# Kernel tuning notes

Measured on AMD Instinct MI355X. Metric: run time of the kernel, lower is better.

## Reference

```python
import jax, jax.numpy as jnp
import numpy as np


def grid_sample_bilinear(feat, grid):
    """Bilinear grid_sample, align_corners=False, zeros padding.
    feat: [B, C, H, W]; grid: [B, N, 2] with (x, y) in [-1, 1]. Returns [B, C, N].
    """
    B, C, H, W = feat.shape
    gx, gy = grid[..., 0], grid[..., 1]
    # unnormalize (align_corners=False): pixel = ((g + 1) * size - 1) / 2
    ix = ((gx + 1.0) * W - 1.0) * 0.5
    iy = ((gy + 1.0) * H - 1.0) * 0.5
    x0 = jnp.floor(ix)
    y0 = jnp.floor(iy)
    x1 = x0 + 1.0
    y1 = y0 + 1.0
    wx1 = ix - x0
    wx0 = 1.0 - wx1
    wy1 = iy - y0
    wy0 = 1.0 - wy1
    featf = feat.reshape(B, C, H * W)

    def corner(xi, yi, w):
        valid = (xi >= 0) & (xi <= W - 1) & (yi >= 0) & (yi <= H - 1)
        xi_c = jnp.clip(xi, 0, W - 1).astype(jnp.int32)
        yi_c = jnp.clip(yi, 0, H - 1).astype(jnp.int32)
        idx = yi_c * W + xi_c                                  # [B, N]
        vals = jnp.take_along_axis(featf, idx[:, None, :], axis=2)  # [B, C, N]
        return vals * (w * valid.astype(feat.dtype))[:, None, :]

    return (corner(x0, y0, wx0 * wy0) + corner(x1, y0, wx1 * wy0)
            + corner(x0, y1, wx0 * wy1) + corner(x1, y1, wx1 * wy1))


def setup_inputs() -> dict:
    key = jax.random.key(0)
    ks = jax.random.split(key, 8)
    B_T, C, H, W = 128, 256, 64, 64
    J = 17
    n_heads, n_points = 8, 4
    HP = n_heads * n_points
    video_features = jax.random.normal(ks[0], (B_T, C, H, W), dtype=jnp.float32)
    reference_points = jax.random.uniform(ks[1], (B_T, J, 2), dtype=jnp.float32,
                                          minval=-1.0, maxval=1.0)
    # offset predictor: Linear(C -> HP*2); weights init small like the module
    W_off = 0.01 * jax.random.normal(ks[2], (C, HP * 2), dtype=jnp.float32)
    b_off = 0.01 * jax.random.normal(ks[3], (HP * 2,), dtype=jnp.float32)
    # weight predictor: Linear(C -> HP)
    W_w = 0.01 * jax.random.normal(ks[4], (C, HP), dtype=jnp.float32)
    b_w = jnp.zeros((HP,), dtype=jnp.float32)
    # output projection: Linear(C -> C), xavier-ish scale
    W_out = jax.random.normal(ks[5], (C, C), dtype=jnp.float32) * (1.0 / np.sqrt(C))
    b_out = jnp.zeros((C,), dtype=jnp.float32)
    return {"video_features": video_features, "reference_points": reference_points,
            "W_off": W_off, "b_off": b_off, "W_w": W_w, "b_w": b_w,
            "W_out": W_out, "b_out": b_out}


def reference(video_features, reference_points, W_off, b_off, W_w, b_w, W_out, b_out):
    B, C, H, W = video_features.shape
    J = reference_points.shape[1]
    HP = W_w.shape[1]  # n_heads * n_points
    # initial queries: sample features at reference points -> [B, J, C]
    q = grid_sample_bilinear(video_features, reference_points).transpose(0, 2, 1)
    # learned fractional offsets: [B, J, HP, 2]
    offsets = (q @ W_off + b_off).reshape(B, J, HP, 2)
    # softmax attention weights over all heads*points: [B, J, HP]
    weights = jax.nn.softmax(q @ W_w + b_w, axis=-1)
    # final sampling grid, clamped to valid range: [B, J*HP, 2]
    grid = jnp.clip(reference_points[:, :, None, :] + offsets, -1.0, 1.0)
    grid = grid.reshape(B, J * HP, 2)
    # sample and weighted-sum: [B, C, J, HP] x [B, J, HP] -> [B, J, C]
    sampled = grid_sample_bilinear(video_features, grid).reshape(B, C, J, HP)
    out = jnp.einsum('bcjp,bjp->bjc', sampled, weights)
    return out @ W_out + b_out
```

## Files before the change

### kernel.cpp

```cpp
#include <hip/hip_runtime.h>

#define B_  128
#define C_  256
#define H_  64
#define W_  64
#define J_  17
#define HP_ 32
#define HW_ (H_ * W_)
#define CG_ 2
#define GBLK_ 2048
#define NTASK (B_ * (C_ / CG_))
#define TASKS_PER_BLK (NTASK / GBLK_)
#define PROJ_ROWS 8

__global__ __launch_bounds__(256)
void pass12_kernel(const float* __restrict__ feat,
                   const float* __restrict__ refpts,
                   const float* __restrict__ Woff,
                   const float* __restrict__ boff,
                   const float* __restrict__ Ww,
                   const float* __restrict__ bw,
                   int4*  __restrict__ meta_idx,
                   float4* __restrict__ meta_w)
{
    __shared__ float q_lds[C_];
    __shared__ float part_off[4][64];
    __shared__ float part_w[8][32];
    __shared__ float off_lds[2 * HP_];
    __shared__ float logit_lds[HP_];

    const int bj = blockIdx.x;
    const int b  = bj / J_;
    const int j  = bj % J_;
    const int c  = threadIdx.x;

    const float rx = refpts[(b * J_ + j) * 2 + 0];
    const float ry = refpts[(b * J_ + j) * 2 + 1];

    {
        const float* featbc = feat + (size_t)(b * C_ + c) * HW_;
        float ix = (rx + 1.0f) * (0.5f * W_) - 0.5f;
        float iy = (ry + 1.0f) * (0.5f * H_) - 0.5f;
        float x0f = floorf(ix), y0f = floorf(iy);
        int x0 = (int)x0f, y0 = (int)y0f;
        int x1 = x0 + 1,  y1 = y0 + 1;
        float wx1 = ix - x0f, wx0 = 1.0f - wx1;
        float wy1 = iy - y0f, wy0 = 1.0f - wy1;
        bool vx0 = (x0 >= 0) && (x0 < W_);
        bool vx1 = (x1 >= 0) && (x1 < W_);
        bool vy0 = (y0 >= 0) && (y0 < H_);
        bool vy1 = (y1 >= 0) && (y1 < H_);
        int x0c = min(max(x0, 0), W_ - 1), x1c = min(max(x1, 0), W_ - 1);
        int y0c = min(max(y0, 0), H_ - 1), y1c = min(max(y1, 0), H_ - 1);
        float v00 = (vx0 && vy0) ? featbc[y0c * W_ + x0c] : 0.0f;
        float v10 = (vx1 && vy0) ? featbc[y0c * W_ + x1c] : 0.0f;
        float v01 = (vx0 && vy1) ? featbc[y1c * W_ + x0c] : 0.0f;
        float v11 = (vx1 && vy1) ? featbc[y1c * W_ + x1c] : 0.0f;
        q_lds[c] = v00 * (wx0 * wy0) + v10 * (wx1 * wy0)
                 + v01 * (wx0 * wy1) + v11 * (wx1 * wy1);
    }
    __syncthreads();

    {
        const int wv = c >> 6, ln = c & 63;
        float aoff = 0.0f;
        #pragma unroll 8
        for (int i = 0; i < 64; ++i) {
            const int k = wv * 64 + i;
            aoff += q_lds[k] * Woff[k * 64 + ln];
        }
        part_off[wv][ln] = aoff;
        const int h = ln >> 5, p = ln & 31;
        float aw = 0.0f;
        #pragma unroll 8
        for (int i = 0; i < 32; ++i) {
            const int k = wv * 64 + h * 32 + i;
            aw += q_lds[k] * Ww[k * 32 + p];
        }
        part_w[wv * 2 + h][p] = aw;
    }
    __syncthreads();
    if (c < 64) {
        off_lds[c] = boff[c] + part_off[0][c] + part_off[1][c]
                   + part_off[2][c] + part_off[3][c];
    } else if (c < 96) {
        const int p = c - 64;
        float s = bw[p];
        #pragma unroll
        for (int sidx = 0; sidx < 8; ++sidx) s += part_w[sidx][p];
        logit_lds[p] = s;
    }
    __syncthreads();

    if (c < HP_) {
        float l = logit_lds[c];
        float m = l;
        #pragma unroll
        for (int mask = 16; mask >= 1; mask >>= 1) m = fmaxf(m, __shfl_xor(m, mask));
        float e = expf(l - m);
        float s = e;
        #pragma unroll
        for (int mask = 16; mask >= 1; mask >>= 1) s += __shfl_xor(s, mask);
        const float ww = e / s;

        float gx = fminf(fmaxf(rx + off_lds[2 * c + 0], -1.0f), 1.0f);
        float gy = fminf(fmaxf(ry + off_lds[2 * c + 1], -1.0f), 1.0f);
        float ix = (gx + 1.0f) * (0.5f * W_) - 0.5f;
        float iy = (gy + 1.0f) * (0.5f * H_) - 0.5f;
        float x0f = floorf(ix), y0f = floorf(iy);
        int x0 = (int)x0f, y0 = (int)y0f;
        int x1 = x0 + 1,  y1 = y0 + 1;
        float wx1 = ix - x0f, wx0 = 1.0f - wx1;
        float wy1 = iy - y0f, wy0 = 1.0f - wy1;
        float v00 = (float)((x0 >= 0) && (x0 < W_) && (y0 >= 0) && (y0 < H_));
        float v10 = (float)((x1 >= 0) && (x1 < W_) && (y0 >= 0) && (y0 < H_));
        float v01 = (float)((x0 >= 0) && (x0 < W_) && (y1 >= 0) && (y1 < H_));
        float v11 = (float)((x1 >= 0) && (x1 < W_) && (y1 >= 0) && (y1 < H_));
        int x0c = min(max(x0, 0), W_ - 1), x1c = min(max(x1, 0), W_ - 1);
        int y0c = min(max(y0, 0), H_ - 1), y1c = min(max(y1, 0), H_ - 1);
        const int mi = bj * HP_ + c;
        meta_idx[mi] = make_int4(y0c * W_ + x0c, y0c * W_ + x1c,
                                 y1c * W_ + x0c, y1c * W_ + x1c);
        meta_w[mi] = make_float4(ww * wx0 * wy0 * v00, ww * wx1 * wy0 * v10,
                                 ww * wx0 * wy1 * v01, ww * wx1 * wy1 * v11);
    }
}

__device__ __forceinline__ void stage_task(const float* __restrict__ feat,
                                           int task, float* buf, int t) {
    const int b   = task >> 7;
    const int cgp = task & 127;
    const int wv  = t >> 6;
    const int ln  = t & 63;
    const char* gsrc = (const char*)(feat + (size_t)(b * C_ + cgp * CG_) * HW_);
    #pragma unroll
    for (int i = 0; i < 8; ++i) {
        const size_t off = ((size_t)(i * 256 + wv * 64)) * 16;
        __builtin_amdgcn_global_load_lds(
            (const __attribute__((address_space(1))) void*)(gsrc + off + (size_t)ln * 16),
            (__attribute__((address_space(3))) void*)((char*)buf + off),
            16, 0, 0);
    }
}

__global__ __launch_bounds__(256)
void gather_kernel(const float* __restrict__ feat,
                   const int4*  __restrict__ meta_idx,
                   const float4* __restrict__ meta_w,
                   float* __restrict__ acc)
{
    __shared__ float lds[2 * CG_ * HW_];

    const int blk = blockIdx.x;
    const int t   = threadIdx.x;
    const int wv  = t >> 6;
    const int ln  = t & 63;
    const int p    = ln & 31;
    const int half = ln >> 5;

    const int task0 = blk * TASKS_PER_BLK;

    stage_task(feat, task0, lds, t);
    __syncthreads();

    #pragma unroll 1
    for (int r = 0; r < TASKS_PER_BLK; ++r) {
        const int task = task0 + r;
        const int b    = task >> 7;
        const int c0   = (task & 127) * CG_;
        float* cur = lds + (r & 1) * (CG_ * HW_);

        int4   id_r[3];
        float4 w_r[3];
        #pragma unroll
        for (int iter = 0; iter < 3; ++iter) {
            const int j = iter * 8 + wv * 2 + half;
            if (j < J_) {
                const int mi = (b * J_ + j) * HP_ + p;
                id_r[iter] = meta_idx[mi];
                w_r[iter]  = meta_w[mi];
            } else {
                id_r[iter] = make_int4(0, 0, 0, 0);
                w_r[iter]  = make_float4(0.f, 0.f, 0.f, 0.f);
            }
        }
        __builtin_amdgcn_sched_barrier(0);

        if (r + 1 < TASKS_PER_BLK)
            stage_task(feat, task + 1, lds + ((r + 1) & 1) * (CG_ * HW_), t);
        __builtin_amdgcn_sched_barrier(0);

        #pragma unroll
        for (int iter = 0; iter < 3; ++iter) {
            const int j = iter * 8 + wv * 2 + half;
            const int4   id = id_r[iter];
            const float4 w  = w_r[iter];
            float pj0 = w.x * cur[id.x] + w.y * cur[id.y]
                      + w.z * cur[id.z] + w.w * cur[id.w];
            float pj1 = w.x * cur[HW_ + id.x] + w.y * cur[HW_ + id.y]
                      + w.z * cur[HW_ + id.z] + w.w * cur[HW_ + id.w];
            #pragma unroll
            for (int mask = 16; mask >= 1; mask >>= 1) {
                pj0 += __shfl_xor(pj0, mask);
                pj1 += __shfl_xor(pj1, mask);
            }
            if (j < J_ && p == 0) {
                float2* dst = (float2*)(acc + ((size_t)(b * J_ + j)) * C_ + c0);
                *dst = make_float2(pj0, pj1);
            }
        }

        __syncthreads();
    }
}

__global__ __launch_bounds__(256)
void proj_kernel(const float* __restrict__ acc,
                 const float* __restrict__ Wout,
                 const float* __restrict__ bout,
                 float* __restrict__ out)
{
    __shared__ float a_lds[PROJ_ROWS][C_];
    const int bj0 = blockIdx.x * PROJ_ROWS;
    const int t   = threadIdx.x;

    #pragma unroll
    for (int r = 0; r < PROJ_ROWS; ++r)
        a_lds[r][t] = acc[(size_t)(bj0 + r) * C_ + t];
    __syncthreads();

    float o[PROJ_ROWS];
    const float bb = bout[t];
    #pragma unroll
    for (int r = 0; r < PROJ_ROWS; ++r) o[r] = bb;
    #pragma unroll 4
    for (int k = 0; k < C_; ++k) {
        const float wvv = Wout[(size_t)k * C_ + t];
        #pragma unroll
        for (int r = 0; r < PROJ_ROWS; ++r)
            o[r] += a_lds[r][k] * wvv;
    }
    #pragma unroll
    for (int r = 0; r < PROJ_ROWS; ++r)
        out[(size_t)(bj0 + r) * C_ + t] = o[r];
}

extern "C" void kernel_launch(void* const* d_in, const int* in_sizes, int n_in,
                              void* d_out, int out_size, void* d_ws, size_t ws_size,
                              hipStream_t stream) {
    const float* feat   = (const float*)d_in[0];
    const float* refpts = (const float*)d_in[1];
    const float* Woff   = (const float*)d_in[2];
    const float* boff   = (const float*)d_in[3];
    const float* Ww     = (const float*)d_in[4];
    const float* bw     = (const float*)d_in[5];
    const float* Wout   = (const float*)d_in[6];
    const float* bout   = (const float*)d_in[7];
    float* out = (float*)d_out;

    const size_t n_meta    = (size_t)B_ * J_ * HP_;
    const size_t idx_bytes = n_meta * sizeof(int4);
    const size_t w_bytes   = n_meta * sizeof(float4);

    char* ws = (char*)d_ws;
    int4*   meta_idx = (int4*)ws;
    float4* meta_w   = (float4*)(ws + idx_bytes);
    float*  acc      = (float*)(ws + idx_bytes + w_bytes);

    pass12_kernel<<<dim3(B_ * J_), dim3(256), 0, stream>>>(
        feat, refpts, Woff, boff, Ww, bw, meta_idx, meta_w);
    gather_kernel<<<dim3(GBLK_), dim3(256), 0, stream>>>(
        feat, meta_idx, meta_w, acc);
    proj_kernel<<<dim3((B_ * J_) / PROJ_ROWS), dim3(256), 0, stream>>>(
        acc, Wout, bout, out);
}
```

Measured before the change: 180.2 us.

## Replace persistent double-buffered gather with one-shot blocks staging four channel planes

The gather kernel no longer loops over several tasks per block with a double-buffered LDS prefetch. Each 512-thread block now stages four channel planes (64 KB) into LDS once, gathers the four corners for all joints, and writes a float4 per joint. Overlap now comes from having multiple resident blocks per CU rather than from an explicit software pipeline. This removes the per-task barrier and staging logic, but relies on occupancy with large LDS footprints to hide load latency.

```diff
diff --git a/kernel.cpp b/kernel.cpp
--- a/kernel.cpp
+++ b/kernel.cpp
@@ -7,10 +7,7 @@
 #define J_  17
 #define HP_ 32
 #define HW_ (H_ * W_)
-#define CG_ 2
-#define GBLK_ 2048
-#define NTASK (B_ * (C_ / CG_))
-#define TASKS_PER_BLK (NTASK / GBLK_)
+#define CG_ 4
 #define PROJ_ROWS 8
 
 __global__ __launch_bounds__(256)
@@ -126,91 +123,80 @@
     }
 }
 
-__device__ __forceinline__ void stage_task(const float* __restrict__ feat,
-                                           int task, float* buf, int t) {
-    const int b   = task >> 7;
-    const int cgp = task & 127;
-    const int wv  = t >> 6;
-    const int ln  = t & 63;
-    const char* gsrc = (const char*)(feat + (size_t)(b * C_ + cgp * CG_) * HW_);
-    #pragma unroll
-    for (int i = 0; i < 8; ++i) {
-        const size_t off = ((size_t)(i * 256 + wv * 64)) * 16;
-        __builtin_amdgcn_global_load_lds(
-            (const __attribute__((address_space(1))) void*)(gsrc + off + (size_t)ln * 16),
-            (__attribute__((address_space(3))) void*)((char*)buf + off),
-            16, 0, 0);
-    }
-}
-
-__global__ __launch_bounds__(256)
+__global__ __launch_bounds__(512, 2)
 void gather_kernel(const float* __restrict__ feat,
                    const int4*  __restrict__ meta_idx,
                    const float4* __restrict__ meta_w,
                    float* __restrict__ acc)
 {
-    __shared__ float lds[2 * CG_ * HW_];
+    __shared__ float plane[CG_ * HW_];
 
     const int blk = blockIdx.x;
+    const int b   = blk >> 6;
+    const int cg  = blk & 63;
+    const int c0  = cg * CG_;
     const int t   = threadIdx.x;
     const int wv  = t >> 6;
     const int ln  = t & 63;
+
+    {
+        const char* gsrc = (const char*)(feat + (size_t)(b * C_ + c0) * HW_);
+        #pragma unroll
+        for (int i = 0; i < 8; ++i) {
+            const size_t off = ((size_t)(i * 512 + wv * 64)) * 16;
+            __builtin_amdgcn_global_load_lds(
+                (const __attribute__((address_space(1))) void*)(gsrc + off + (size_t)ln * 16),
+                (__attribute__((address_space(3))) void*)((char*)plane + off),
+                16, 0, 0);
+        }
+    }
+
     const int p    = ln & 31;
     const int half = ln >> 5;
-
-    const int task0 = blk * TASKS_PER_BLK;
-
-    stage_task(feat, task0, lds, t);
-    __syncthreads();
-
-    #pragma unroll 1
-    for (int r = 0; r < TASKS_PER_BLK; ++r) {
-        const int task = task0 + r;
-        const int b    = task >> 7;
-        const int c0   = (task & 127) * CG_;
-        float* cur = lds + (r & 1) * (CG_ * HW_);
-
-        int4   id_r[3];
-        float4 w_r[3];
-        #pragma unroll
-        for (int iter = 0; iter < 3; ++iter) {
-            const int j = iter * 8 + wv * 2 + half;
+    int4   id_r[2];
+    float4 w_r[2];
+    #pragma unroll
+    for (int iter = 0; iter < 2; ++iter) {
+        const int jbase = iter * 16 + wv * 2;
+        id_r[iter] = make_int4(0, 0, 0, 0);
+        w_r[iter]  = make_float4(0.f, 0.f, 0.f, 0.f);
+        if (jbase < J_) {
+            const int j = jbase + half;
             if (j < J_) {
                 const int mi = (b * J_ + j) * HP_ + p;
                 id_r[iter] = meta_idx[mi];
                 w_r[iter]  = meta_w[mi];
-            } else {
-                id_r[iter] = make_int4(0, 0, 0, 0);
-                w_r[iter]  = make_float4(0.f, 0.f, 0.f, 0.f);
             }
         }
-        __builtin_amdgcn_sched_barrier(0);
-
-        if (r + 1 < TASKS_PER_BLK)
-            stage_task(feat, task + 1, lds + ((r + 1) & 1) * (CG_ * HW_), t);
-        __builtin_amdgcn_sched_barrier(0);
-
-        #pragma unroll
-        for (int iter = 0; iter < 3; ++iter) {
-            const int j = iter * 8 + wv * 2 + half;
-            const int4   id = id_r[iter];
-            const float4 w  = w_r[iter];
-            float pj0 = w.x * cur[id.x] + w.y * cur[id.y]
-                      + w.z * cur[id.z] + w.w * cur[id.w];
-            float pj1 = w.x * cur[HW_ + id.x] + w.y * cur[HW_ + id.y]
-                      + w.z * cur[HW_ + id.z] + w.w * cur[HW_ + id.w];
-            #pragma unroll
-            for (int mask = 16; mask >= 1; mask >>= 1) {
-                pj0 += __shfl_xor(pj0, mask);
-                pj1 += __shfl_xor(pj1, mask);
-            }
-            if (j < J_ && p == 0) {
-                float2* dst = (float2*)(acc + ((size_t)(b * J_ + j)) * C_ + c0);
-                *dst = make_float2(pj0, pj1);
-            }
-        }
-
-        __syncthreads();
+    }
+    __syncthreads();
+
+    #pragma unroll
+    for (int iter = 0; iter < 2; ++iter) {
+        const int jbase = iter * 16 + wv * 2;
+        if (jbase >= J_) continue;
+        const int j = jbase + half;
+        const int4   id = id_r[iter];
+        const float4 w  = w_r[iter];
+        float pj0 = w.x * plane[0 * HW_ + id.x] + w.y * plane[0 * HW_ + id.y]
+                  + w.z * plane[0 * HW_ + id.z] + w.w * plane[0 * HW_ + id.w];
+        float pj1 = w.x * plane[1 * HW_ + id.x] + w.y * plane[1 * HW_ + id.y]
+                  + w.z * plane[1 * HW_ + id.z] + w.w * plane[1 * HW_ + id.w];
+        float pj2 = w.x * plane[2 * HW_ + id.x] + w.y * plane[2 * HW_ + id.y]
+                  + w.z * plane[2 * HW_ + id.z] + w.w * plane[2 * HW_ + id.w];
+        float pj3 = w.x * plane[3 * HW_ + id.x] + w.y * plane[3 * HW_ + id.y]
+                  + w.z * plane[3 * HW_ + id.z] + w.w * plane[3 * HW_ + id.w];
+        #pragma unroll
+        for (int mask = 16; mask >= 1; mask >>= 1) {
+            pj0 += __shfl_xor(pj0, mask);
+            pj1 += __shfl_xor(pj1, mask);
+            pj2 += __shfl_xor(pj2, mask);
+            pj3 += __shfl_xor(pj3, mask);
+        }
+        if (j < J_ && p == 0) {
+            float4* dst = (float4*)(acc + ((size_t)(b * J_ + j)) * C_ + c0);
+            *dst = make_float4(pj0, pj1, pj2, pj3);
+        }
     }
 }
 
@@ -269,7 +255,7 @@
 
     pass12_kernel<<<dim3(B_ * J_), dim3(256), 0, stream>>>(
         feat, refpts, Woff, boff, Ww, bw, meta_idx, meta_w);
-    gather_kernel<<<dim3(GBLK_), dim3(256), 0, stream>>>(
+    gather_kernel<<<dim3(B_ * (C_ / CG_)), dim3(512), 0, stream>>>(
         feat, meta_idx, meta_w, acc);
     proj_kernel<<<dim3((B_ * J_) / PROJ_ROWS), dim3(256), 0, stream>>>(
         acc, Wout, bout, out);
```

After: 154.8 us. -14.1%, faster.
